# Kernel tuning notes

Measured on AMD Instinct MI355X. Metric: run time of the kernel, lower is better.

## Reference

```python
import jax, jax.numpy as jnp
import numpy as np

B, L, V, H, NL = 128, 512, 2048, 512, 2


def setup_inputs() -> dict:
    key = jax.random.key(0)
    ks = jax.random.split(key, 20)
    s = 0.05  # param scale
    inp = {
        "input_ids": jax.random.randint(ks[0], (B,), 0, V),
        "last_hidden": jax.random.normal(ks[1], (NL, B, H), jnp.float32),
        "word_dict_vec": jax.random.normal(ks[2], (B, V, H), jnp.float32),
        "encoder_outputs": jax.random.normal(ks[3], (L, B, H), jnp.float32),
        "seq_mask": (jax.random.uniform(ks[4], (B, L)) < 0.2).at[:, 0].set(False),
        # Attn params (torch Linear: y = x @ W.T + b)
        "attn_W": jax.random.normal(ks[5], (H, 2 * H), jnp.float32) * s,
        "attn_b": jax.random.normal(ks[6], (H,), jnp.float32) * s,
        "score_W": jax.random.normal(ks[7], (1, H), jnp.float32) * s,
        # concat layer
        "concat_W": jax.random.normal(ks[8], (H, 2 * H), jnp.float32) * s,
        "concat_b": jax.random.normal(ks[9], (H,), jnp.float32) * s,
        # GRU layer 0 (input 2H) and layer 1 (input H); gates ordered r,z,n as in torch
        "W_ih0": jax.random.normal(ks[10], (3 * H, 2 * H), jnp.float32) * s,
        "W_hh0": jax.random.normal(ks[11], (3 * H, H), jnp.float32) * s,
        "b_ih0": jax.random.normal(ks[12], (3 * H,), jnp.float32) * s,
        "b_hh0": jax.random.normal(ks[13], (3 * H,), jnp.float32) * s,
        "W_ih1": jax.random.normal(ks[14], (3 * H, H), jnp.float32) * s,
        "W_hh1": jax.random.normal(ks[15], (3 * H, H), jnp.float32) * s,
        "b_ih1": jax.random.normal(ks[16], (3 * H,), jnp.float32) * s,
        "b_hh1": jax.random.normal(ks[17], (3 * H,), jnp.float32) * s,
    }
    return inp


def _gru_cell(x, h, W_ih, W_hh, b_ih, b_hh):
    gi = x @ W_ih.T + b_ih
    gh = h @ W_hh.T + b_hh
    i_r, i_z, i_n = jnp.split(gi, 3, axis=-1)
    h_r, h_z, h_n = jnp.split(gh, 3, axis=-1)
    r = jax.nn.sigmoid(i_r + h_r)
    z = jax.nn.sigmoid(i_z + h_z)
    n = jnp.tanh(i_n + r * h_n)
    return (1.0 - z) * n + z * h


def reference(input_ids, last_hidden, word_dict_vec, encoder_outputs, seq_mask,
              attn_W, attn_b, score_W, concat_W, concat_b,
              W_ih0, W_hh0, b_ih0, b_hh0, W_ih1, W_hh1, b_ih1, b_hh1):
    # one_hot @ word_dict_vec == per-batch row gather (same math)
    emb = word_dict_vec[jnp.arange(B), input_ids]  # [B, H]

    # Bahdanau additive attention over encoder_outputs [L, B, H]
    q = last_hidden[-1]  # [B, H]
    hid = jnp.broadcast_to(q[None], (L, B, H))
    energy_in = jnp.concatenate([hid, encoder_outputs], axis=2)  # [L, B, 2H]
    e = jnp.tanh(energy_in @ attn_W.T + attn_b) @ score_W.T      # [L, B, 1]
    scores = e[..., 0].T                                          # [B, L]
    scores = jnp.where(seq_mask, jnp.float32(-1e12), scores)
    aw = jax.nn.softmax(scores, axis=1)                           # [B, L]

    context = jnp.einsum('bl,lbh->bh', aw, encoder_outputs)       # [B, H]

    # single-step 2-layer GRU (eval mode: dropout = identity)
    x0 = jnp.concatenate([emb, context], axis=1)                  # [B, 2H]
    h0 = _gru_cell(x0, last_hidden[0], W_ih0, W_hh0, b_ih0, b_hh0)
    h1 = _gru_cell(h0, last_hidden[1], W_ih1, W_hh1, b_ih1, b_hh1)
    hidden = jnp.stack([h0, h1])                                  # [2, B, H]

    output = jnp.tanh(jnp.concatenate([h1, context], axis=1) @ concat_W.T + concat_b)
    return output, hidden
```

## Files before the change

### kernel.cpp

```cpp
#include <hip/hip_runtime.h>
#include <stdint.h>

#define Hdim 512
#define Bdim 128
#define Ldim 512
#define Vdim 2048

typedef unsigned short u16;
using f32x4  = float  __attribute__((ext_vector_type(4)));
using bf16x8 = __bf16 __attribute__((ext_vector_type(8)));

__device__ inline u16 f2bf(float x) {
  uint32_t u = __float_as_uint(x);
  u += 0x7fffu + ((u >> 16) & 1u);
  return (u16)(u >> 16);
}
__device__ inline uint32_t pk2(float lo, float hi) {
  return (uint32_t)f2bf(lo) | ((uint32_t)f2bf(hi) << 16);
}
__device__ inline float fast_tanh(float x) {
  return 1.0f - 2.0f / (__expf(2.0f * x) + 1.0f);
}
__device__ inline float fast_sig(float x) { return 1.0f / (1.0f + __expf(-x)); }

__device__ inline bf16x8 pack_bf8(float4 x, float4 y) {
  union { uint32_t d[4]; bf16x8 v; } r;
  r.d[0] = pk2(x.x, x.y); r.d[1] = pk2(x.z, x.w);
  r.d[2] = pk2(y.x, y.y); r.d[3] = pk2(y.z, y.w);
  return r.v;
}

__global__ __launch_bounds__(512)
void prep_kernel(const float* __restrict__ lh, const float* __restrict__ attn_W,
                 const float* __restrict__ attn_b, const float* __restrict__ cat_W,
                 const float* __restrict__ W_ih0, const float* __restrict__ W_hh0,
                 const float* __restrict__ W_ih1, const float* __restrict__ W_hh1,
                 const float* __restrict__ b_ih0, const float* __restrict__ b_hh0,
                 const float* __restrict__ b_ih1, const float* __restrict__ b_hh1,
                 const float* __restrict__ wdv, const int* __restrict__ ids,
                 const void* __restrict__ mask,
                 float* __restrict__ qW, u16* __restrict__ arena,
                 float* __restrict__ biasg0, float* __restrict__ biasg1,
                 u16* __restrict__ X0bf, u16* __restrict__ X1bf, int* __restrict__ flag) {
  int blk = blockIdx.x, t = threadIdx.x;
  int lane = t & 63, wid = t >> 6;
  int fr = lane & 15, g = lane >> 4, kof = g * 8;

  if (blk < 16) {
    int mh = wid & 3, nh = wid >> 2;
    int n0 = blk * 32 + nh * 16;
    int rb0 = mh * 32;
    f32x4 ac0 = {0.f, 0.f, 0.f, 0.f}, ac1 = {0.f, 0.f, 0.f, 0.f};
    const float* q = lh + 65536;
#pragma unroll 2
    for (int kt = 0; kt < 512; kt += 32) {
      const float* qr0 = q + (size_t)(rb0 + fr) * 512 + kt + kof;
      const float* qr1 = qr0 + 16 * 512;
      const float* wr  = attn_W + (size_t)(n0 + fr) * 1024 + kt + kof;
      float4 x0 = *(const float4*)qr0, x1 = *(const float4*)(qr0 + 4);
      float4 y0 = *(const float4*)qr1, y1 = *(const float4*)(qr1 + 4);
      float4 w0 = *(const float4*)wr,  w1 = *(const float4*)(wr + 4);
      bf16x8 A0 = pack_bf8(x0, x1), A1 = pack_bf8(y0, y1), Bb = pack_bf8(w0, w1);
      ac0 = __builtin_amdgcn_mfma_f32_16x16x32_bf16(A0, Bb, ac0, 0, 0, 0);
      ac1 = __builtin_amdgcn_mfma_f32_16x16x32_bf16(A1, Bb, ac1, 0, 0, 0);
    }
    float vb = attn_b[n0 + fr];
#pragma unroll
    for (int j = 0; j < 4; ++j) {
      qW[(size_t)(rb0 + g * 4 + j) * 512 + n0 + fr]      = ac0[j] + vb;
      qW[(size_t)(rb0 + 16 + g * 4 + j) * 512 + n0 + fr] = ac1[j] + vb;
    }
    return;
  }
  if (blk == 16) {
    __shared__ int sf;
    if (t == 0) sf = 0;
    __syncthreads();
    const uint32_t* m32 = (const uint32_t*)mask;
    int found = 0;
    for (int i = t; i < 16384; i += 512)
      if (m32[i] & 0xffffff00u) found = 1;
    if (found) sf = 1;
    __syncthreads();
    if (t == 0) *flag = sf;
    return;
  }
  const int ARENA_Q = 1507328;
  int i = (blk - 17) * 512 + t;
  if (i < ARENA_Q) {
    int e = i * 4;
    float4 v = {0.f, 0.f, 0.f, 0.f};
    if (e < 262144) {
      int o = e >> 9, k = e & 511;
      v = *(const float4*)(attn_W + (size_t)o * 1024 + 512 + k);
    } else if (e < 786432) {
      int e2 = e - 262144; int o = e2 >> 10, k = e2 & 1023;
      v = *(const float4*)(cat_W + (size_t)o * 1024 + k);
    } else if (e < 3932160) {
      int e2 = e - 786432; int row = e2 / 1536, k = e2 % 1536;
      int o = row >> 2, gt = row & 3;
      if (gt == 0)      v = (k < 1024) ? *(const float4*)(W_ih0 + (size_t)o * 1024 + k)
                                       : *(const float4*)(W_hh0 + (size_t)o * 512 + k - 1024);
      else if (gt == 1) v = (k < 1024) ? *(const float4*)(W_ih0 + (size_t)(512 + o) * 1024 + k)
                                       : *(const float4*)(W_hh0 + (size_t)(512 + o) * 512 + k - 1024);
      else if (gt == 2) { if (k < 1024)  v = *(const float4*)(W_ih0 + (size_t)(1024 + o) * 1024 + k); }
      else              { if (k >= 1024) v = *(const float4*)(W_hh0 + (size_t)(1024 + o) * 512 + k - 1024); }
    } else {
      int e2 = e - 3932160; int row = e2 >> 10, k = e2 & 1023;
      int o = row >> 2, gt = row & 3;
      if (gt == 0)      v = (k < 512) ? *(const float4*)(W_ih1 + (size_t)o * 512 + k)
                                      : *(const float4*)(W_hh1 + (size_t)o * 512 + k - 512);
      else if (gt == 1) v = (k < 512) ? *(const float4*)(W_ih1 + (size_t)(512 + o) * 512 + k)
                                      : *(const float4*)(W_hh1 + (size_t)(512 + o) * 512 + k - 512);
      else if (gt == 2) { if (k < 512)  v = *(const float4*)(W_ih1 + (size_t)(1024 + o) * 512 + k); }
      else              { if (k >= 512) v = *(const float4*)(W_hh1 + (size_t)(1024 + o) * 512 + k - 512); }
    }
    ushort4 u;
    u.x = f2bf(v.x); u.y = f2bf(v.y); u.z = f2bf(v.z); u.w = f2bf(v.w);
    *(ushort4*)(arena + e) = u;
    return;
  }
  int i2 = i - ARENA_Q;
  if (i2 < 1024) {
    int r4 = i2 * 4; int layer = r4 >> 11; int r = r4 & 2047; int o = r >> 2;
    const float* bi = layer ? b_ih1 : b_ih0;
    const float* bh = layer ? b_hh1 : b_hh0;
    float4 v;
    v.x = bi[o] + bh[o];
    v.y = bi[512 + o] + bh[512 + o];
    v.z = bi[1024 + o];
    v.w = bh[1024 + o];
    *(float4*)((layer ? biasg1 : biasg0) + r) = v;
  } else if (i2 < 1024 + 16384) {
    int j = (i2 - 1024) * 4; int b = j >> 9, i0 = j & 511;
    float4 v = *(const float4*)(wdv + (size_t)b * (Vdim * Hdim) + (size_t)ids[b] * 512 + i0);
    ushort4 u;
    u.x = f2bf(v.x); u.y = f2bf(v.y); u.z = f2bf(v.z); u.w = f2bf(v.w);
    *(ushort4*)(X0bf + b * 1536 + i0) = u;
  } else if (i2 < 1024 + 32768) {
    int j = (i2 - 1024 - 16384) * 4; int b = j >> 9, i0 = j & 511;
    float4 v = *(const float4*)(lh + (size_t)b * 512 + i0);
    ushort4 u;
    u.x = f2bf(v.x); u.y = f2bf(v.y); u.z = f2bf(v.z); u.w = f2bf(v.w);
    *(ushort4*)(X0bf + b * 1536 + 1024 + i0) = u;
  } else if (i2 < 1024 + 49152) {
    int j = (i2 - 1024 - 32768) * 4; int b = j >> 9, i0 = j & 511;
    float4 v = *(const float4*)(lh + 65536 + (size_t)b * 512 + i0);
    ushort4 u;
    u.x = f2bf(v.x); u.y = f2bf(v.y); u.z = f2bf(v.z); u.w = f2bf(v.w);
    *(ushort4*)(X1bf + b * 1024 + 512 + i0) = u;
  }
}

__global__ __launch_bounds__(512)
void attn_kernel(const float* __restrict__ enc, const u16* __restrict__ Wenc,
                 const float* __restrict__ qW, const float* __restrict__ scW,
                 float* __restrict__ scores) {
  __shared__ __align__(16) u16 As[2][64 * 40];
  __shared__ float part[8 * 64];
  int blk = blockIdx.x, t = threadIdx.x;
  int lane = t & 63, wid = t >> 6;
  int fr = lane & 15, g = lane >> 4, kof = g * 8;
  int l  = blk >> 1;
  int mh = blk & 1;
  const int arow = t >> 3;
  const int aseg = (t & 7) * 4;

  f32x4 acc[4][4];
#pragma unroll
  for (int i = 0; i < 4; ++i)
#pragma unroll
    for (int j = 0; j < 4; ++j) acc[i][j] = (f32x4){0.f, 0.f, 0.f, 0.f};

  const float* abase = enc + ((size_t)l * 128 + mh * 64 + arow) * 512 + aseg;
  const u16* bbase = Wenc + (size_t)(wid * 64 + fr) * 512 + kof;

  float4 ra = *(const float4*)abase;
  bf16x8 cb[4];
#pragma unroll
  for (int ni = 0; ni < 4; ++ni)
    cb[ni] = *(const bf16x8*)(bbase + (size_t)(ni * 16) * 512);

#pragma unroll 2
  for (int step = 0; step < 16; ++step) {
    int sel = step & 1;
    __syncthreads();
    ushort4 ap;
    ap.x = f2bf(ra.x); ap.y = f2bf(ra.y); ap.z = f2bf(ra.z); ap.w = f2bf(ra.w);
    *(ushort4*)(&As[sel][arow * 40 + aseg]) = ap;
    bf16x8 nb[4];
#pragma unroll
    for (int ni = 0; ni < 4; ++ni) nb[ni] = cb[ni];
    if (step < 15) {
      int kt = (step + 1) * 32;
      ra = *(const float4*)(abase + kt);
#pragma unroll
      for (int ni = 0; ni < 4; ++ni)
        nb[ni] = *(const bf16x8*)(bbase + (size_t)(ni * 16) * 512 + kt);
    }
    __syncthreads();
#pragma unroll
    for (int mi = 0; mi < 4; ++mi) {
      bf16x8 av = *(const bf16x8*)(&As[sel][(mi * 16 + fr) * 40 + kof]);
#pragma unroll
      for (int ni = 0; ni < 4; ++ni)
        acc[mi][ni] = __builtin_amdgcn_mfma_f32_16x16x32_bf16(av, cb[ni], acc[mi][ni], 0, 0, 0);
    }
#pragma unroll
    for (int ni = 0; ni < 4; ++ni) cb[ni] = nb[ni];
  }
#pragma unroll
  for (int mi = 0; mi < 4; ++mi) {
    float rs0 = 0.f, rs1 = 0.f, rs2 = 0.f, rs3 = 0.f;
#pragma unroll
    for (int ni = 0; ni < 4; ++ni) {
      int o = wid * 64 + ni * 16 + fr;
      float sw = scW[o];
      int brow = mh * 64 + mi * 16 + g * 4;
      rs0 += sw * fast_tanh(acc[mi][ni][0] + qW[(size_t)(brow + 0) * 512 + o]);
      rs1 += sw * fast_tanh(acc[mi][ni][1] + qW[(size_t)(brow + 1) * 512 + o]);
      rs2 += sw * fast_tanh(acc[mi][ni][2] + qW[(size_t)(brow + 2) * 512 + o]);
      rs3 += sw * fast_tanh(acc[mi][ni][3] + qW[(size_t)(brow + 3) * 512 + o]);
    }
#pragma unroll
    for (int d = 1; d < 16; d <<= 1) {
      rs0 += __shfl_xor(rs0, d);
      rs1 += __shfl_xor(rs1, d);
      rs2 += __shfl_xor(rs2, d);
      rs3 += __shfl_xor(rs3, d);
    }
    if (fr < 4) {
      float v = (fr == 0) ? rs0 : (fr == 1) ? rs1 : (fr == 2) ? rs2 : rs3;
      part[wid * 64 + mi * 16 + g * 4 + fr] = v;
    }
  }
  __syncthreads();
  if (t < 64) {
    float s = 0.f;
#pragma unroll
    for (int w2 = 0; w2 < 8; ++w2) s += part[w2 * 64 + t];
    scores[(size_t)(mh * 64 + t) * 512 + l] = s;
  }
}

__global__ __launch_bounds__(256)
void softctx_kernel(const float* __restrict__ scores, const void* __restrict__ maskp,
                    const int* __restrict__ flag, const float* __restrict__ enc,
                    u16* __restrict__ X0bf, u16* __restrict__ c1bf) {
  __shared__ float wgt[512];
  __shared__ float redm[4], reds[4];
  __shared__ float ps[256 * 2];
  int blk = blockIdx.x, t = threadIdx.x;
  int lane = t & 63, wid = t >> 6;
  int b = blk >> 3, c = blk & 7;
  int l0 = t, l1 = t + 256;
  float s0 = scores[(size_t)b * 512 + l0];
  float s1 = scores[(size_t)b * 512 + l1];
  bool isbyte = (*flag != 0);
  bool m0, m1;
  if (isbyte) {
    m0 = ((const uint8_t*)maskp)[b * 512 + l0] != 0;
    m1 = ((const uint8_t*)maskp)[b * 512 + l1] != 0;
  } else {
    m0 = ((const int*)maskp)[b * 512 + l0] != 0;
    m1 = ((const int*)maskp)[b * 512 + l1] != 0;
  }
  float v0 = m0 ? -1e12f : s0;
  float v1 = m1 ? -1e12f : s1;
  float mx = fmaxf(v0, v1);
#pragma unroll
  for (int d = 1; d < 64; d <<= 1) mx = fmaxf(mx, __shfl_xor(mx, d));
  if (lane == 0) redm[wid] = mx;
  __syncthreads();
  mx = fmaxf(fmaxf(redm[0], redm[1]), fmaxf(redm[2], redm[3]));
  float e0 = __expf(v0 - mx), e1 = __expf(v1 - mx);
  float sm = e0 + e1;
#pragma unroll
  for (int d = 1; d < 64; d <<= 1) sm += __shfl_xor(sm, d);
  if (lane == 0) reds[wid] = sm;
  __syncthreads();
  sm = reds[0] + reds[1] + reds[2] + reds[3];
  float inv = 1.0f / sm;
  wgt[l0] = e0 * inv;
  wgt[l1] = e1 * inv;
  __syncthreads();
  int cp = t & 31, lq = t >> 5;
  int col = c * 64 + cp * 2;
  float a0 = 0.f, a1 = 0.f;
  const float* ebase = enc + (size_t)b * 512 + col;
#pragma unroll 4
  for (int l2 = lq * 64; l2 < lq * 64 + 64; ++l2) {
    float wl = wgt[l2];
    float2 ev = *(const float2*)(ebase + (size_t)l2 * 65536);
    a0 += wl * ev.x;
    a1 += wl * ev.y;
  }
  ps[(lq * 32 + cp) * 2 + 0] = a0;
  ps[(lq * 32 + cp) * 2 + 1] = a1;
  __syncthreads();
  if (t < 32) {
    float r0 = 0.f, r1 = 0.f;
#pragma unroll
    for (int q2 = 0; q2 < 8; ++q2) {
      r0 += ps[(q2 * 32 + t) * 2 + 0];
      r1 += ps[(q2 * 32 + t) * 2 + 1];
    }
    int cc = c * 64 + t * 2;
    uint32_t packed = pk2(r0, r1);
    *(uint32_t*)(X0bf + b * 1536 + 512 + cc) = packed;
    *(uint32_t*)(c1bf + b * 1024 + 512 + cc) = packed;
  }
}

__global__ __launch_bounds__(256)
void gru_gemm_kernel(const u16* __restrict__ X, int ldx, const u16* __restrict__ Wp,
                     const float* __restrict__ biasp, const float* __restrict__ hprev,
                     int K, float* __restrict__ hout, u16* __restrict__ xdst) {
  __shared__ float ct[128][36];
  int n0 = blockIdx.x * 32;
  int t = threadIdx.x, lane = t & 63, w = t >> 6;
  int fr = lane & 15, g = lane >> 4, kof = g * 8;
  f32x4 acc[2][2];
#pragma unroll
  for (int i = 0; i < 2; ++i)
#pragma unroll
    for (int j = 0; j < 2; ++j) acc[i][j] = (f32x4){0.f, 0.f, 0.f, 0.f};
  const u16* Xr0 = X + (size_t)(w * 32 + fr) * ldx;
  const u16* Xr1 = Xr0 + (size_t)16 * ldx;
  const u16* Wr0 = Wp + (size_t)(n0 + fr) * K;
  const u16* Wr1 = Wp + (size_t)(n0 + 16 + fr) * K;
#pragma unroll 4
  for (int kt = 0; kt < K; kt += 32) {
    bf16x8 a0 = *(const bf16x8*)(Xr0 + kt + kof);
    bf16x8 a1 = *(const bf16x8*)(Xr1 + kt + kof);
    bf16x8 b0 = *(const bf16x8*)(Wr0 + kt + kof);
    bf16x8 b1 = *(const bf16x8*)(Wr1 + kt + kof);
    acc[0][0] = __builtin_amdgcn_mfma_f32_16x16x32_bf16(a0, b0, acc[0][0], 0, 0, 0);
    acc[0][1] = __builtin_amdgcn_mfma_f32_16x16x32_bf16(a0, b1, acc[0][1], 0, 0, 0);
    acc[1][0] = __builtin_amdgcn_mfma_f32_16x16x32_bf16(a1, b0, acc[1][0], 0, 0, 0);
    acc[1][1] = __builtin_amdgcn_mfma_f32_16x16x32_bf16(a1, b1, acc[1][1], 0, 0, 0);
  }
#pragma unroll
  for (int mi = 0; mi < 2; ++mi)
#pragma unroll
    for (int ni = 0; ni < 2; ++ni) {
      int col = ni * 16 + fr;
      float vb = biasp[n0 + col];
#pragma unroll
      for (int j = 0; j < 4; ++j)
        ct[w * 32 + 16 * mi + g * 4 + j][col] = acc[mi][ni][j] + vb;
    }
  __syncthreads();
#pragma unroll
  for (int i = 0; i < 4; ++i) {
    int u = t + i * 256;
    int b = u >> 3, ol = u & 7;
    float cr  = ct[b][ol * 4 + 0];
    float cz  = ct[b][ol * 4 + 1];
    float ci  = ct[b][ol * 4 + 2];
    float chh = ct[b][ol * 4 + 3];
    int o = blockIdx.x * 8 + ol;
    float r = fast_sig(cr), z = fast_sig(cz);
    float n = tanhf(ci + r * chh);
    float h = (1.0f - z) * n + z * hprev[b * 512 + o];
    hout[b * 512 + o] = h;
    xdst[b * 1024 + o] = f2bf(h);
  }
}

__global__ __launch_bounds__(256)
void thin_gemm32(const u16* __restrict__ X, int ldx, const u16* __restrict__ W,
                 const float* __restrict__ bias, float* __restrict__ C, int ldc,
                 int K, int act) {
  int n0 = blockIdx.x * 32;
  int t = threadIdx.x, lane = t & 63, w = t >> 6;
  int fr = lane & 15, g = lane >> 4, kof = g * 8;
  f32x4 acc[2][2];
#pragma unroll
  for (int i = 0; i < 2; ++i)
#pragma unroll
    for (int j = 0; j < 2; ++j) acc[i][j] = (f32x4){0.f, 0.f, 0.f, 0.f};
  const u16* Xr0 = X + (size_t)(w * 32 + fr) * ldx;
  const u16* Xr1 = Xr0 + (size_t)16 * ldx;
  const u16* Wr0 = W + (size_t)(n0 + fr) * K;
  const u16* Wr1 = W + (size_t)(n0 + 16 + fr) * K;
#pragma unroll 4
  for (int kt = 0; kt < K; kt += 32) {
    bf16x8 a0 = *(const bf16x8*)(Xr0 + kt + kof);
    bf16x8 a1 = *(const bf16x8*)(Xr1 + kt + kof);
    bf16x8 b0 = *(const bf16x8*)(Wr0 + kt + kof);
    bf16x8 b1 = *(const bf16x8*)(Wr1 + kt + kof);
    acc[0][0] = __builtin_amdgcn_mfma_f32_16x16x32_bf16(a0, b0, acc[0][0], 0, 0, 0);
    acc[0][1] = __builtin_amdgcn_mfma_f32_16x16x32_bf16(a0, b1, acc[0][1], 0, 0, 0);
    acc[1][0] = __builtin_amdgcn_mfma_f32_16x16x32_bf16(a1, b0, acc[1][0], 0, 0, 0);
    acc[1][1] = __builtin_amdgcn_mfma_f32_16x16x32_bf16(a1, b1, acc[1][1], 0, 0, 0);
  }
#pragma unroll
  for (int mi = 0; mi < 2; ++mi)
#pragma unroll
    for (int ni = 0; ni < 2; ++ni) {
      int col = n0 + ni * 16 + fr;
      float vb = bias[col];
#pragma unroll
      for (int j = 0; j < 4; ++j) {
        int row = w * 32 + 16 * mi + g * 4 + j;
        float v = acc[mi][ni][j] + vb;
        if (act) v = tanhf(v);
        C[(size_t)row * ldc + col] = v;
      }
    }
}

extern "C" void kernel_launch(void* const* d_in, const int* in_sizes, int n_in,
                              void* d_out, int out_size, void* d_ws, size_t ws_size,
                              hipStream_t stream) {
  const int*   ids    = (const int*)  d_in[0];
  const float* lh     = (const float*)d_in[1];
  const float* wdv    = (const float*)d_in[2];
  const float* enc    = (const float*)d_in[3];
  const void*  mask   = d_in[4];
  const float* attn_W = (const float*)d_in[5];
  const float* attn_b = (const float*)d_in[6];
  const float* scW    = (const float*)d_in[7];
  const float* cat_W  = (const float*)d_in[8];
  const float* cat_b  = (const float*)d_in[9];
  const float* W_ih0  = (const float*)d_in[10];
  const float* W_hh0  = (const float*)d_in[11];
  const float* b_ih0  = (const float*)d_in[12];
  const float* b_hh0  = (const float*)d_in[13];
  const float* W_ih1  = (const float*)d_in[14];
  const float* W_hh1  = (const float*)d_in[15];
  const float* b_ih1  = (const float*)d_in[16];
  const float* b_hh1  = (const float*)d_in[17];

  float* out = (float*)d_out;
  float* h0  = out + 65536;
  float* h1  = out + 131072;

  float* ws       = (float*)d_ws;
  float* qW       = ws;
  float* scores   = ws + 65536;
  float* biasg0   = ws + 131072;
  float* biasg1   = ws + 133120;
  int*   flag     = (int*)(ws + 135168);
  u16*   arena    = (u16*)(ws + 135184);
  u16*   X0bf     = (u16*)(ws + 3149840);
  u16*   X1bf     = (u16*)(ws + 3248144);
  u16*   c1bf     = (u16*)(ws + 3313680);

  const u16* Wenc = arena;
  const u16* Wcat = arena + 262144;
  const u16* Wg0p = arena + 786432;
  const u16* Wg1p = arena + 3932160;

  prep_kernel<<<3059, 512, 0, stream>>>(lh, attn_W, attn_b, cat_W,
                                        W_ih0, W_hh0, W_ih1, W_hh1,
                                        b_ih0, b_hh0, b_ih1, b_hh1,
                                        wdv, ids, mask,
                                        qW, arena, biasg0, biasg1, X0bf, X1bf, flag);
  attn_kernel<<<1024, 512, 0, stream>>>(enc, Wenc, qW, scW, scores);
  softctx_kernel<<<1024, 256, 0, stream>>>(scores, mask, flag, enc, X0bf, c1bf);
  gru_gemm_kernel<<<64, 256, 0, stream>>>(X0bf, 1536, Wg0p, biasg0, lh, 1536, h0, X1bf);
  gru_gemm_kernel<<<64, 256, 0, stream>>>(X1bf, 1024, Wg1p, biasg1, lh + 65536, 1024, h1, c1bf);
  thin_gemm32<<<16, 256, 0, stream>>>(c1bf, 1024, Wcat, cat_b, out, 512, 1024, 1);
}
```

Before: 186.4 us.

## Merge attention row halves into 1024-thread blocks and split softmax-context wider

The attention GEMM kernel now handles all 128 batch rows of one sequence position per 1024-thread block, instead of two 512-thread blocks each handling 64 rows. Each Wenc tile is therefore loaded once per position rather than twice. The softmax-context kernel now splits each batch row into 16 column chunks instead of 8, doubling the grid for more parallelism; each block recomputes the softmax, so the mask and score reads are repeated per chunk. bf16 conversion switches from manual bit rounding to native __bf16 casts and vector converts, and waves-per-EU is pinned at 4, which caps registers for the larger block.

New measurement: 196.1 us. 5.2% more time.

```diff
diff --git a/kernel.cpp b/kernel.cpp
--- a/kernel.cpp
+++ b/kernel.cpp
@@ -8,15 +8,19 @@
 
 typedef unsigned short u16;
 using f32x4  = float  __attribute__((ext_vector_type(4)));
+using f32x8  = float  __attribute__((ext_vector_type(8)));
 using bf16x8 = __bf16 __attribute__((ext_vector_type(8)));
+using bf16x2 = __bf16 __attribute__((ext_vector_type(2)));
+using bf16x4 = __bf16 __attribute__((ext_vector_type(4)));
 
 __device__ inline u16 f2bf(float x) {
-  uint32_t u = __float_as_uint(x);
-  u += 0x7fffu + ((u >> 16) & 1u);
-  return (u16)(u >> 16);
+  __bf16 b = (__bf16)x;
+  union { __bf16 b; u16 u; } c; c.b = b; return c.u;
 }
 __device__ inline uint32_t pk2(float lo, float hi) {
-  return (uint32_t)f2bf(lo) | ((uint32_t)f2bf(hi) << 16);
+  union { bf16x2 v; uint32_t u; } c;
+  c.v[0] = (__bf16)lo; c.v[1] = (__bf16)hi;
+  return c.u;
 }
 __device__ inline float fast_tanh(float x) {
   return 1.0f - 2.0f / (__expf(2.0f * x) + 1.0f);
@@ -24,10 +28,8 @@
 __device__ inline float fast_sig(float x) { return 1.0f / (1.0f + __expf(-x)); }
 
 __device__ inline bf16x8 pack_bf8(float4 x, float4 y) {
-  union { uint32_t d[4]; bf16x8 v; } r;
-  r.d[0] = pk2(x.x, x.y); r.d[1] = pk2(x.z, x.w);
-  r.d[2] = pk2(y.x, y.y); r.d[3] = pk2(y.z, y.w);
-  return r.v;
+  f32x8 f = {x.x, x.y, x.z, x.w, y.x, y.y, y.z, y.w};
+  return __builtin_convertvector(f, bf16x8);
 }
 
 __global__ __launch_bounds__(512)
@@ -152,19 +154,19 @@
   }
 }
 
-__global__ __launch_bounds__(512)
+__global__ __launch_bounds__(1024)
+__attribute__((amdgpu_waves_per_eu(4, 4)))
 void attn_kernel(const float* __restrict__ enc, const u16* __restrict__ Wenc,
                  const float* __restrict__ qW, const float* __restrict__ scW,
                  float* __restrict__ scores) {
-  __shared__ __align__(16) u16 As[2][64 * 40];
-  __shared__ float part[8 * 64];
-  int blk = blockIdx.x, t = threadIdx.x;
+  __shared__ __align__(16) u16 As[2][128 * 40];
+  __shared__ float part[16 * 64];
+  int l = blockIdx.x, t = threadIdx.x;
   int lane = t & 63, wid = t >> 6;
   int fr = lane & 15, g = lane >> 4, kof = g * 8;
-  int l  = blk >> 1;
-  int mh = blk & 1;
+  int mg = wid & 1, og = wid >> 1;
   const int arow = t >> 3;
-  const int aseg = (t & 7) * 4;
+  const int aks = (t & 7) * 4;
 
   f32x4 acc[4][4];
 #pragma unroll
@@ -172,10 +174,10 @@
 #pragma unroll
     for (int j = 0; j < 4; ++j) acc[i][j] = (f32x4){0.f, 0.f, 0.f, 0.f};
 
-  const float* abase = enc + ((size_t)l * 128 + mh * 64 + arow) * 512 + aseg;
-  const u16* bbase = Wenc + (size_t)(wid * 64 + fr) * 512 + kof;
-
-  float4 ra = *(const float4*)abase;
+  const float* abase = enc + ((size_t)l * 128 + arow) * 512 + aks;
+  const u16* bbase = Wenc + (size_t)(og * 64 + fr) * 512 + kof;
+
+  float4 pA = *(const float4*)abase;
   bf16x8 cb[4];
 #pragma unroll
   for (int ni = 0; ni < 4; ++ni)
@@ -185,15 +187,17 @@
   for (int step = 0; step < 16; ++step) {
     int sel = step & 1;
     __syncthreads();
-    ushort4 ap;
-    ap.x = f2bf(ra.x); ap.y = f2bf(ra.y); ap.z = f2bf(ra.z); ap.w = f2bf(ra.w);
-    *(ushort4*)(&As[sel][arow * 40 + aseg]) = ap;
+    {
+      f32x4 fv = {pA.x, pA.y, pA.z, pA.w};
+      bf16x4 bv = __builtin_convertvector(fv, bf16x4);
+      *(bf16x4*)(&As[sel][arow * 40 + aks]) = bv;
+    }
     bf16x8 nb[4];
 #pragma unroll
     for (int ni = 0; ni < 4; ++ni) nb[ni] = cb[ni];
     if (step < 15) {
       int kt = (step + 1) * 32;
-      ra = *(const float4*)(abase + kt);
+      pA = *(const float4*)(abase + kt);
 #pragma unroll
       for (int ni = 0; ni < 4; ++ni)
         nb[ni] = *(const bf16x8*)(bbase + (size_t)(ni * 16) * 512 + kt);
@@ -201,7 +205,7 @@
     __syncthreads();
 #pragma unroll
     for (int mi = 0; mi < 4; ++mi) {
-      bf16x8 av = *(const bf16x8*)(&As[sel][(mi * 16 + fr) * 40 + kof]);
+      bf16x8 av = *(const bf16x8*)(&As[sel][(mg * 64 + mi * 16 + fr) * 40 + kof]);
 #pragma unroll
       for (int ni = 0; ni < 4; ++ni)
         acc[mi][ni] = __builtin_amdgcn_mfma_f32_16x16x32_bf16(av, cb[ni], acc[mi][ni], 0, 0, 0);
@@ -214,9 +218,9 @@
     float rs0 = 0.f, rs1 = 0.f, rs2 = 0.f, rs3 = 0.f;
 #pragma unroll
     for (int ni = 0; ni < 4; ++ni) {
-      int o = wid * 64 + ni * 16 + fr;
+      int o = og * 64 + ni * 16 + fr;
       float sw = scW[o];
-      int brow = mh * 64 + mi * 16 + g * 4;
+      int brow = mg * 64 + mi * 16 + g * 4;
       rs0 += sw * fast_tanh(acc[mi][ni][0] + qW[(size_t)(brow + 0) * 512 + o]);
       rs1 += sw * fast_tanh(acc[mi][ni][1] + qW[(size_t)(brow + 1) * 512 + o]);
       rs2 += sw * fast_tanh(acc[mi][ni][2] + qW[(size_t)(brow + 2) * 512 + o]);
@@ -235,16 +239,17 @@
     }
   }
   __syncthreads();
-  if (t < 64) {
+  if (t < 128) {
+    int mg2 = t >> 6, r64 = t & 63;
     float s = 0.f;
 #pragma unroll
-    for (int w2 = 0; w2 < 8; ++w2) s += part[w2 * 64 + t];
-    scores[(size_t)(mh * 64 + t) * 512 + l] = s;
+    for (int o2 = 0; o2 < 8; ++o2) s += part[(o2 * 2 + mg2) * 64 + r64];
+    scores[(size_t)t * 512 + l] = s;
   }
 }
 
 __global__ __launch_bounds__(256)
-void softctx_kernel(const float* __restrict__ scores, const void* __restrict__ maskp,
+void softctx_kernel(const float* __restrict__ sp, const void* __restrict__ maskp,
                     const int* __restrict__ flag, const float* __restrict__ enc,
                     u16* __restrict__ X0bf, u16* __restrict__ c1bf) {
   __shared__ float wgt[512];
@@ -252,10 +257,10 @@
   __shared__ float ps[256 * 2];
   int blk = blockIdx.x, t = threadIdx.x;
   int lane = t & 63, wid = t >> 6;
-  int b = blk >> 3, c = blk & 7;
+  int b = blk >> 4, c = blk & 15;
   int l0 = t, l1 = t + 256;
-  float s0 = scores[(size_t)b * 512 + l0];
-  float s1 = scores[(size_t)b * 512 + l1];
+  float s0 = sp[(size_t)b * 512 + l0];
+  float s1 = sp[(size_t)b * 512 + l1];
   bool isbyte = (*flag != 0);
   bool m0, m1;
   if (isbyte) {
@@ -284,28 +289,28 @@
   wgt[l0] = e0 * inv;
   wgt[l1] = e1 * inv;
   __syncthreads();
-  int cp = t & 31, lq = t >> 5;
-  int col = c * 64 + cp * 2;
+  int cp = t & 15, lq = t >> 4;
+  int col = c * 32 + cp * 2;
   float a0 = 0.f, a1 = 0.f;
   const float* ebase = enc + (size_t)b * 512 + col;
 #pragma unroll 4
-  for (int l2 = lq * 64; l2 < lq * 64 + 64; ++l2) {
+  for (int l2 = lq * 32; l2 < lq * 32 + 32; ++l2) {
     float wl = wgt[l2];
     float2 ev = *(const float2*)(ebase + (size_t)l2 * 65536);
     a0 += wl * ev.x;
     a1 += wl * ev.y;
   }
-  ps[(lq * 32 + cp) * 2 + 0] = a0;
-  ps[(lq * 32 + cp) * 2 + 1] = a1;
-  __syncthreads();
-  if (t < 32) {
+  ps[(lq * 16 + cp) * 2 + 0] = a0;
+  ps[(lq * 16 + cp) * 2 + 1] = a1;
+  __syncthreads();
+  if (t < 16) {
     float r0 = 0.f, r1 = 0.f;
 #pragma unroll
-    for (int q2 = 0; q2 < 8; ++q2) {
-      r0 += ps[(q2 * 32 + t) * 2 + 0];
-      r1 += ps[(q2 * 32 + t) * 2 + 1];
-    }
-    int cc = c * 64 + t * 2;
+    for (int q2 = 0; q2 < 16; ++q2) {
+      r0 += ps[(q2 * 16 + t) * 2 + 0];
+      r1 += ps[(q2 * 16 + t) * 2 + 1];
+    }
+    int cc = c * 32 + t * 2;
     uint32_t packed = pk2(r0, r1);
     *(uint32_t*)(X0bf + b * 1536 + 512 + cc) = packed;
     *(uint32_t*)(c1bf + b * 1024 + 512 + cc) = packed;
@@ -437,16 +442,16 @@
   float* h0  = out + 65536;
   float* h1  = out + 131072;
 
-  float* ws       = (float*)d_ws;
-  float* qW       = ws;
-  float* scores   = ws + 65536;
-  float* biasg0   = ws + 131072;
-  float* biasg1   = ws + 133120;
-  int*   flag     = (int*)(ws + 135168);
-  u16*   arena    = (u16*)(ws + 135184);
-  u16*   X0bf     = (u16*)(ws + 3149840);
-  u16*   X1bf     = (u16*)(ws + 3248144);
-  u16*   c1bf     = (u16*)(ws + 3313680);
+  float* ws     = (float*)d_ws;
+  float* qW     = ws;
+  float* scores = ws + 65536;
+  float* biasg0 = ws + 131072;
+  float* biasg1 = ws + 133120;
+  int*   flag   = (int*)(ws + 135168);
+  u16*   arena  = (u16*)(ws + 135184);
+  u16*   X0bf   = (u16*)(ws + 3149840);
+  u16*   X1bf   = (u16*)(ws + 3248144);
+  u16*   c1bf   = (u16*)(ws + 3313680);
 
   const u16* Wenc = arena;
   const u16* Wcat = arena + 262144;
@@ -458,8 +463,8 @@
                                         b_ih0, b_hh0, b_ih1, b_hh1,
                                         wdv, ids, mask,
                                         qW, arena, biasg0, biasg1, X0bf, X1bf, flag);
-  attn_kernel<<<1024, 512, 0, stream>>>(enc, Wenc, qW, scW, scores);
-  softctx_kernel<<<1024, 256, 0, stream>>>(scores, mask, flag, enc, X0bf, c1bf);
+  attn_kernel<<<512, 1024, 0, stream>>>(enc, Wenc, qW, scW, scores);
+  softctx_kernel<<<2048, 256, 0, stream>>>(scores, mask, flag, enc, X0bf, c1bf);
   gru_gemm_kernel<<<64, 256, 0, stream>>>(X0bf, 1536, Wg0p, biasg0, lh, 1536, h0, X1bf);
   gru_gemm_kernel<<<64, 256, 0, stream>>>(X1bf, 1024, Wg1p, biasg1, lh + 65536, 1024, h1, c1bf);
   thin_gemm32<<<16, 256, 0, stream>>>(c1bf, 1024, Wcat, cat_b, out, 512, 1024, 1);
```
